# Kernel optimization log

Measured on AMD Instinct MI355X. Metric: run time of the kernel, lower is better.

Reference implementation:

```python
import jax, jax.numpy as jnp
import numpy as np

C_LEN, Q_LEN, D = 8192, 1024, 1024  # D = 2*hidden_size


def setup_inputs() -> dict:
    key = jax.random.key(0)
    ks = jax.random.split(key, 5)
    scale = 1.0 / np.sqrt(D)
    return {
        "H": jax.random.normal(ks[0], (C_LEN, D), dtype=jnp.float32),
        "U": jax.random.normal(ks[1], (Q_LEN, D), dtype=jnp.float32),
        "w_q": jax.random.normal(ks[2], (D,), dtype=jnp.float32) * scale,
        "b_q": jnp.zeros((1,), dtype=jnp.float32),
        "w_c": jax.random.normal(ks[3], (D,), dtype=jnp.float32) * scale,
        "b_c": jnp.zeros((1,), dtype=jnp.float32),
        "w_qc": jax.random.normal(ks[4], (D,), dtype=jnp.float32) * scale,
        "b_qc": jnp.zeros((1,), dtype=jnp.float32),
    }


def reference(H, U, w_q, b_q, w_c, b_c, w_qc, b_qc):
    # Per-token loop qc[:, i] = (H * U[i]) @ w_qc + b_qc collapses to one GEMM:
    # qc[j, i] = sum_k H[j,k] * w_qc[k] * U[i,k] + b_qc
    qc = jnp.einsum("cd,qd->cq", H * w_qc, U) + b_qc          # [c_len, q_len]
    q_term = (U @ w_q + b_q)[None, :]                          # [1, q_len]
    c_term = (H @ w_c + b_c)[:, None]                          # [c_len, 1]
    s = qc + q_term + c_term                                    # [c_len, q_len]
    q2c_atten = jax.nn.softmax(s, axis=0)                       # softmax over context dim (as written)
    U_toggler = q2c_atten @ U                                   # [c_len, D]
    b = jnp.max(H, axis=1)                                      # [c_len]
    c2q_atten = jax.nn.softmax(b)                               # [c_len]
    H_toggler = jnp.broadcast_to((c2q_atten @ H)[None, :], (H.shape[0], H.shape[1]))
    return (U_toggler, H_toggler)
```

## Files before the change

### kernel.cpp

```cpp
#include <hip/hip_runtime.h>

#define C_LEN 8192
#define Q_LEN 1024
#define DDIM  1024

typedef __attribute__((ext_vector_type(8))) short short8;
typedef __attribute__((ext_vector_type(4))) float f32x4;

static __device__ __forceinline__ unsigned short f2bf(float f){
  unsigned u = __float_as_uint(f);
  unsigned rounding = 0x7fffu + ((u >> 16) & 1u);
  return (unsigned short)((u + rounding) >> 16);
}

static __device__ __forceinline__ void async_copy16(const void* g, void* l){
  __builtin_amdgcn_global_load_lds(
      (const __attribute__((address_space(1))) void*)g,
      (__attribute__((address_space(3))) void*)l, 16, 0, 0);
}

static __device__ __forceinline__ float waveRedSum(float v){
  #pragma unroll
  for(int o=32;o;o>>=1) v += __shfl_down(v,o);
  return v;
}
static __device__ __forceinline__ float waveRedMax(float v){
  #pragma unroll
  for(int o=32;o;o>>=1) v = fmaxf(v,__shfl_down(v,o));
  return v;
}

__global__ void prep_H(const float* __restrict__ H, const float* __restrict__ w_qc,
                       const float* __restrict__ w_c, const float* __restrict__ b_c,
                       unsigned short* __restrict__ Abf, float* __restrict__ c_term,
                       float* __restrict__ eb){
  const int c = blockIdx.x, t = threadIdx.x;
  float4 h   = reinterpret_cast<const float4*>(H + (size_t)c*DDIM)[t];
  float4 wqc = reinterpret_cast<const float4*>(w_qc)[t];
  float4 wc  = reinterpret_cast<const float4*>(w_c)[t];
  float dot = h.x*wc.x + h.y*wc.y + h.z*wc.z + h.w*wc.w;
  float mx  = fmaxf(fmaxf(h.x,h.y), fmaxf(h.z,h.w));
  ushort4 o;
  o.x=f2bf(h.x*wqc.x); o.y=f2bf(h.y*wqc.y); o.z=f2bf(h.z*wqc.z); o.w=f2bf(h.w*wqc.w);
  reinterpret_cast<ushort4*>(Abf)[(size_t)c*256 + t] = o;
  __shared__ float sd[4], sm[4];
  int w=t>>6, l=t&63;
  dot = waveRedSum(dot); mx = waveRedMax(mx);
  if(l==0){ sd[w]=dot; sm[w]=mx; }
  __syncthreads();
  if(t==0){
    c_term[c] = sd[0]+sd[1]+sd[2]+sd[3] + b_c[0];
    float m = fmaxf(fmaxf(sm[0],sm[1]), fmaxf(sm[2],sm[3]));
    eb[c] = __expf(m);
  }
}

__global__ void sum_eb(const float* __restrict__ eb, float* __restrict__ btot){
  __shared__ float red[16];
  int t = threadIdx.x, w = t>>6, l = t&63;
  float s = eb[t] + eb[t + 1024] + eb[t + 2048] + eb[t + 3072]
          + eb[t + 4096] + eb[t + 5120] + eb[t + 6144] + eb[t + 7168];
  s = waveRedSum(s);
  if(!l) red[w] = s;
  __syncthreads();
  if(t==0){ float tot=0.f; for(int i=0;i<16;i++) tot+=red[i]; btot[0]=tot; }
}

__global__ void prep_U(const float* __restrict__ U, const float* __restrict__ w_q,
                       const float* __restrict__ b_q, unsigned short* __restrict__ Ubf,
                       float* __restrict__ q_term){
  const int qr = blockIdx.x, t = threadIdx.x;
  float4 u  = reinterpret_cast<const float4*>(U + (size_t)qr*DDIM)[t];
  float4 wq = reinterpret_cast<const float4*>(w_q)[t];
  float dot = u.x*wq.x + u.y*wq.y + u.z*wq.z + u.w*wq.w;
  ushort4 o; o.x=f2bf(u.x); o.y=f2bf(u.y); o.z=f2bf(u.z); o.w=f2bf(u.w);
  reinterpret_cast<ushort4*>(Ubf)[(size_t)qr*256 + t] = o;
  __shared__ float sd[4];
  int w=t>>6, l=t&63;
  dot = waveRedSum(dot);
  if(l==0) sd[w]=dot;
  __syncthreads();
  if(t==0) q_term[qr] = sd[0]+sd[1]+sd[2]+sd[3] + b_q[0];
}

__global__ void transpose_scale_U(const float* __restrict__ U, const float* __restrict__ csum,
                                  unsigned short* __restrict__ Ut){
  __shared__ float tile[64][65];
  const int t = threadIdx.x;
  const int q0 = blockIdx.y*64, d0 = blockIdx.x*64;
  #pragma unroll
  for(int i=0;i<16;i++){
    int idx = i*256 + t, r = idx>>6, col = idx&63;
    tile[r][col] = U[(size_t)(q0+r)*DDIM + d0 + col];
  }
  float inv = 1.f / csum[q0 + (t&63)];
  __syncthreads();
  #pragma unroll
  for(int i=0;i<16;i++){
    int idx = i*256 + t, r = idx>>6, col = idx&63;
    Ut[(size_t)(d0+r)*Q_LEN + q0 + col] = f2bf(tile[col][r] * inv);
  }
}

template<int FUSE_EXP>
__global__ __launch_bounds__(256)
void gemm_bt(const unsigned short* __restrict__ A, const unsigned short* __restrict__ B,
             void* __restrict__ Cout, int M, int N, int K,
             const float* __restrict__ rowAdd, const float* __restrict__ colAdd,
             const float* __restrict__ addC, float* __restrict__ csum){
  __shared__ unsigned short As[2][128][32];
  __shared__ unsigned short Bs[2][128][32];
  const int t = threadIdx.x;
  const int lane = t & 63, wave = t >> 6;
  const int wm = wave & 1, wn = wave >> 1;
  const int lr = lane & 15, quad = lane >> 4;
  const int bm = blockIdx.x * 128, bn = blockIdx.y * 128;
  const int srow = wave*32 + (lane>>2);
  const int skcol = (lane&3)*8;

  f32x4 acc[4][4];
  #pragma unroll
  for(int i=0;i<4;i++)
    #pragma unroll
    for(int j=0;j<4;j++) acc[i][j] = (f32x4){0.f,0.f,0.f,0.f};

  const unsigned short* gA = A + (size_t)(bm + srow)*K + skcol;
  const unsigned short* gB = B + (size_t)(bn + srow)*K + skcol;
  unsigned short* lA[2] = { &As[0][srow][skcol], &As[1][srow][skcol] };
  unsigned short* lB[2] = { &Bs[0][srow][skcol], &Bs[1][srow][skcol] };

  async_copy16(gA,                lA[0]);
  async_copy16(gA + (size_t)16*K, lA[0] + 16*32);
  async_copy16(gB,                lB[0]);
  async_copy16(gB + (size_t)16*K, lB[0] + 16*32);
  gA += 32; gB += 32;

  const int ITERS = K >> 5;
  for(int k=0;k<ITERS;k++){
    const int cur = k & 1, nxt = cur ^ 1;
    __syncthreads();
    if(k+1 < ITERS){
      async_copy16(gA,                lA[nxt]);
      async_copy16(gA + (size_t)16*K, lA[nxt] + 16*32);
      async_copy16(gB,                lB[nxt]);
      async_copy16(gB + (size_t)16*K, lB[nxt] + 16*32);
      gA += 32; gB += 32;
    }
    short8 af[4], bfr[4];
    #pragma unroll
    for(int i=0;i<4;i++){
      af[i]  = *reinterpret_cast<const short8*>(&As[cur][wm*64 + i*16 + lr][quad*8]);
      bfr[i] = *reinterpret_cast<const short8*>(&Bs[cur][wn*64 + i*16 + lr][quad*8]);
    }
    #pragma unroll
    for(int i=0;i<4;i++)
      #pragma unroll
      for(int j=0;j<4;j++)
        acc[i][j] = __builtin_amdgcn_mfma_f32_16x16x32_bf16(af[i], bfr[j], acc[i][j], 0,0,0);
  }

  const int col0 = bn + wn*64;
  if(FUSE_EXP){
    unsigned short* P = (unsigned short*)Cout;
    const float ac = addC[0];
    float cs[4];
    #pragma unroll
    for(int j=0;j<4;j++) cs[j] = 0.f;
    #pragma unroll
    for(int i=0;i<4;i++){
      int row0 = bm + wm*64 + i*16 + quad*4;
      float ra0 = rowAdd[row0], ra1 = rowAdd[row0+1], ra2 = rowAdd[row0+2], ra3 = rowAdd[row0+3];
      #pragma unroll
      for(int j=0;j<4;j++){
        int col = col0 + j*16 + lr;
        float cadd = colAdd[col] + ac;
        float e0 = __expf(acc[i][j][0] + ra0 + cadd);
        float e1 = __expf(acc[i][j][1] + ra1 + cadd);
        float e2 = __expf(acc[i][j][2] + ra2 + cadd);
        float e3 = __expf(acc[i][j][3] + ra3 + cadd);
        P[(size_t)(row0  )*N + col] = f2bf(e0);
        P[(size_t)(row0+1)*N + col] = f2bf(e1);
        P[(size_t)(row0+2)*N + col] = f2bf(e2);
        P[(size_t)(row0+3)*N + col] = f2bf(e3);
        cs[j] += e0+e1+e2+e3;
      }
    }
    #pragma unroll
    for(int j=0;j<4;j++){
      float v = cs[j];
      v += __shfl_xor(v, 16);
      v += __shfl_xor(v, 32);
      if(quad==0) atomicAdd(&csum[col0 + j*16 + lr], v);
    }
  } else {
    float* C = (float*)Cout;
    #pragma unroll
    for(int i=0;i<4;i++){
      int row0 = bm + wm*64 + i*16 + quad*4;
      #pragma unroll
      for(int j=0;j<4;j++){
        int col = col0 + j*16 + lr;
        #pragma unroll
        for(int r=0;r<4;r++)
          C[(size_t)(row0+r)*N + col] = acc[i][j][r];
      }
    }
  }
}

__global__ void h_weighted(const float* __restrict__ H, const float* __restrict__ eb,
                           const float* __restrict__ btot, float* __restrict__ Hrow){
  int d  = blockIdx.x*256 + threadIdx.x;
  int c0 = blockIdx.y*256;
  float acc = 0.f;
  for(int c=c0;c<c0+256;c++)
    acc += eb[c] * H[(size_t)c*DDIM + d];
  atomicAdd(&Hrow[d], acc * (1.f/btot[0]));
}

__global__ void bcast_H(const float* __restrict__ Hrow, float4* __restrict__ out4){
  int gid = blockIdx.x*256 + threadIdx.x;
  int d4 = gid & 255;
  out4[gid] = reinterpret_cast<const float4*>(Hrow)[d4];
}

extern "C" void kernel_launch(void* const* d_in, const int* in_sizes, int n_in,
                              void* d_out, int out_size, void* d_ws, size_t ws_size,
                              hipStream_t stream){
  const float* H    = (const float*)d_in[0];
  const float* U    = (const float*)d_in[1];
  const float* w_q  = (const float*)d_in[2];
  const float* b_q  = (const float*)d_in[3];
  const float* w_c  = (const float*)d_in[4];
  const float* b_c  = (const float*)d_in[5];
  const float* w_qc = (const float*)d_in[6];
  const float* b_qc = (const float*)d_in[7];
  float* out = (float*)d_out;
  char*  ws  = (char*)d_ws;

  unsigned short* P    = (unsigned short*)(ws);
  unsigned short* Abf  = (unsigned short*)(ws + 16777216);
  unsigned short* Ubf  = (unsigned short*)(ws + 33554432);
  unsigned short* Utb  = (unsigned short*)(ws + 35651584);
  char* stats = ws + 37748736;
  float* csum  = (float*)(stats);
  float* Hrow  = (float*)(stats + 4096);
  float* btot  = (float*)(stats + 8192);
  float* cterm = (float*)(stats + 12288);
  float* eb    = (float*)(stats + 45056);
  float* qterm = (float*)(stats + 77824);

  hipMemsetAsync(stats, 0, 8192, stream);

  prep_H<<<C_LEN, 256, 0, stream>>>(H, w_qc, w_c, b_c, Abf, cterm, eb);
  prep_U<<<Q_LEN, 256, 0, stream>>>(U, w_q, b_q, Ubf, qterm);

  gemm_bt<1><<<dim3(64,8), 256, 0, stream>>>(Abf, Ubf, (void*)P, C_LEN, Q_LEN, DDIM,
                                             cterm, qterm, b_qc, csum);

  transpose_scale_U<<<dim3(16,16), 256, 0, stream>>>(U, csum, Utb);

  gemm_bt<0><<<dim3(64,8), 256, 0, stream>>>(P, Utb, (void*)out, C_LEN, DDIM, Q_LEN,
                                             nullptr, nullptr, nullptr, nullptr);

  sum_eb    <<<1, 1024, 0, stream>>>(eb, btot);
  h_weighted<<<dim3(4,32), 256, 0, stream>>>(H, eb, btot, Hrow);
  bcast_H   <<<8192, 256, 0, stream>>>(Hrow, (float4*)(out + (size_t)C_LEN*DDIM));
}
```

Measured before the change: 177.0 us.

## Fuse prep kernels, drop memset and atomics, fold H broadcast into second GEMM

Merges prep_H and prep_U into one launch that also zeroes csum, which removes the memset. It replaces the atomic H-weighted reduction with partial sums plus a combine kernel that also computes the softmax denominator. The broadcast of the H_toggler row now happens in the epilogue of the second GEMM instead of a separate kernel. GEMM tiles are remapped so neighbouring blocks land on the same XCD for L2 reuse. The result is fewer launches and fewer passes over the output, at the cost of a heavier GEMM epilogue.

```diff
diff --git a/kernel.cpp b/kernel.cpp
--- a/kernel.cpp
+++ b/kernel.cpp
@@ -30,57 +30,75 @@
   return v;
 }
 
-__global__ void prep_H(const float* __restrict__ H, const float* __restrict__ w_qc,
-                       const float* __restrict__ w_c, const float* __restrict__ b_c,
-                       unsigned short* __restrict__ Abf, float* __restrict__ c_term,
-                       float* __restrict__ eb){
-  const int c = blockIdx.x, t = threadIdx.x;
-  float4 h   = reinterpret_cast<const float4*>(H + (size_t)c*DDIM)[t];
-  float4 wqc = reinterpret_cast<const float4*>(w_qc)[t];
-  float4 wc  = reinterpret_cast<const float4*>(w_c)[t];
-  float dot = h.x*wc.x + h.y*wc.y + h.z*wc.z + h.w*wc.w;
-  float mx  = fmaxf(fmaxf(h.x,h.y), fmaxf(h.z,h.w));
-  ushort4 o;
-  o.x=f2bf(h.x*wqc.x); o.y=f2bf(h.y*wqc.y); o.z=f2bf(h.z*wqc.z); o.w=f2bf(h.w*wqc.w);
-  reinterpret_cast<ushort4*>(Abf)[(size_t)c*256 + t] = o;
+__global__ void prep_HU(const float* __restrict__ H, const float* __restrict__ U,
+                        const float* __restrict__ w_qc, const float* __restrict__ w_c,
+                        const float* __restrict__ b_c, const float* __restrict__ w_q,
+                        const float* __restrict__ b_q,
+                        unsigned short* __restrict__ Abf, float* __restrict__ cterm,
+                        float* __restrict__ eb, unsigned short* __restrict__ Ubf,
+                        float* __restrict__ qterm, float* __restrict__ csum){
+  const int b = blockIdx.x, t = threadIdx.x;
   __shared__ float sd[4], sm[4];
-  int w=t>>6, l=t&63;
-  dot = waveRedSum(dot); mx = waveRedMax(mx);
-  if(l==0){ sd[w]=dot; sm[w]=mx; }
-  __syncthreads();
-  if(t==0){
-    c_term[c] = sd[0]+sd[1]+sd[2]+sd[3] + b_c[0];
-    float m = fmaxf(fmaxf(sm[0],sm[1]), fmaxf(sm[2],sm[3]));
-    eb[c] = __expf(m);
-  }
-}
-
-__global__ void sum_eb(const float* __restrict__ eb, float* __restrict__ btot){
-  __shared__ float red[16];
+  const int w = t>>6, l = t&63;
+  if(b < C_LEN){
+    float4 h   = reinterpret_cast<const float4*>(H + (size_t)b*DDIM)[t];
+    float4 wqc = reinterpret_cast<const float4*>(w_qc)[t];
+    float4 wc  = reinterpret_cast<const float4*>(w_c)[t];
+    float dot = h.x*wc.x + h.y*wc.y + h.z*wc.z + h.w*wc.w;
+    float mx  = fmaxf(fmaxf(h.x,h.y), fmaxf(h.z,h.w));
+    ushort4 o;
+    o.x=f2bf(h.x*wqc.x); o.y=f2bf(h.y*wqc.y); o.z=f2bf(h.z*wqc.z); o.w=f2bf(h.w*wqc.w);
+    reinterpret_cast<ushort4*>(Abf)[(size_t)b*256 + t] = o;
+    dot = waveRedSum(dot); mx = waveRedMax(mx);
+    if(l==0){ sd[w]=dot; sm[w]=mx; }
+    __syncthreads();
+    if(t==0){
+      cterm[b] = sd[0]+sd[1]+sd[2]+sd[3] + b_c[0];
+      float m = fmaxf(fmaxf(sm[0],sm[1]), fmaxf(sm[2],sm[3]));
+      eb[b] = __expf(m);
+    }
+  } else {
+    const int qr = b - C_LEN;
+    float4 u  = reinterpret_cast<const float4*>(U + (size_t)qr*DDIM)[t];
+    float4 wq = reinterpret_cast<const float4*>(w_q)[t];
+    float dot = u.x*wq.x + u.y*wq.y + u.z*wq.z + u.w*wq.w;
+    ushort4 o; o.x=f2bf(u.x); o.y=f2bf(u.y); o.z=f2bf(u.z); o.w=f2bf(u.w);
+    reinterpret_cast<ushort4*>(Ubf)[(size_t)qr*256 + t] = o;
+    dot = waveRedSum(dot);
+    if(l==0) sd[w]=dot;
+    __syncthreads();
+    if(t==0){
+      qterm[qr] = sd[0]+sd[1]+sd[2]+sd[3] + b_q[0];
+      csum[qr]  = 0.f;
+    }
+  }
+}
+
+__global__ void h_weighted(const float* __restrict__ H, const float* __restrict__ eb,
+                           float* __restrict__ Hpart){
+  int d  = blockIdx.x*256 + threadIdx.x;
+  int cb = blockIdx.y, c0 = cb*256;
+  float acc = 0.f;
+  for(int c=c0;c<c0+256;c++)
+    acc += eb[c] * H[(size_t)c*DDIM + d];
+  Hpart[cb*DDIM + d] = acc;
+}
+
+__global__ void combine_Hrow(const float* __restrict__ Hpart, const float* __restrict__ eb,
+                             float* __restrict__ Hrow){
+  __shared__ float red[4];
   int t = threadIdx.x, w = t>>6, l = t&63;
-  float s = eb[t] + eb[t + 1024] + eb[t + 2048] + eb[t + 3072]
-          + eb[t + 4096] + eb[t + 5120] + eb[t + 6144] + eb[t + 7168];
+  float s = 0.f;
+  for(int i=t;i<C_LEN;i+=256) s += eb[i];
   s = waveRedSum(s);
   if(!l) red[w] = s;
   __syncthreads();
-  if(t==0){ float tot=0.f; for(int i=0;i<16;i++) tot+=red[i]; btot[0]=tot; }
-}
-
-__global__ void prep_U(const float* __restrict__ U, const float* __restrict__ w_q,
-                       const float* __restrict__ b_q, unsigned short* __restrict__ Ubf,
-                       float* __restrict__ q_term){
-  const int qr = blockIdx.x, t = threadIdx.x;
-  float4 u  = reinterpret_cast<const float4*>(U + (size_t)qr*DDIM)[t];
-  float4 wq = reinterpret_cast<const float4*>(w_q)[t];
-  float dot = u.x*wq.x + u.y*wq.y + u.z*wq.z + u.w*wq.w;
-  ushort4 o; o.x=f2bf(u.x); o.y=f2bf(u.y); o.z=f2bf(u.z); o.w=f2bf(u.w);
-  reinterpret_cast<ushort4*>(Ubf)[(size_t)qr*256 + t] = o;
-  __shared__ float sd[4];
-  int w=t>>6, l=t&63;
-  dot = waveRedSum(dot);
-  if(l==0) sd[w]=dot;
-  __syncthreads();
-  if(t==0) q_term[qr] = sd[0]+sd[1]+sd[2]+sd[3] + b_q[0];
+  float btot = red[0]+red[1]+red[2]+red[3];
+  int d = blockIdx.x*256 + t;
+  float acc = 0.f;
+  #pragma unroll
+  for(int p=0;p<32;p++) acc += Hpart[p*DDIM + d];
+  Hrow[d] = acc / btot;
 }
 
 __global__ void transpose_scale_U(const float* __restrict__ U, const float* __restrict__ csum,
@@ -107,14 +125,18 @@
 void gemm_bt(const unsigned short* __restrict__ A, const unsigned short* __restrict__ B,
              void* __restrict__ Cout, int M, int N, int K,
              const float* __restrict__ rowAdd, const float* __restrict__ colAdd,
-             const float* __restrict__ addC, float* __restrict__ csum){
+             const float* __restrict__ addC, float* __restrict__ csum,
+             const float* __restrict__ Hrow, float* __restrict__ outH){
   __shared__ unsigned short As[2][128][32];
   __shared__ unsigned short Bs[2][128][32];
   const int t = threadIdx.x;
   const int lane = t & 63, wave = t >> 6;
   const int wm = wave & 1, wn = wave >> 1;
   const int lr = lane & 15, quad = lane >> 4;
-  const int bm = blockIdx.x * 128, bn = blockIdx.y * 128;
+  const int L = blockIdx.x + (blockIdx.y << 6);
+  const int xcd = L & 7, r = L >> 3;
+  const int by = r & 7, bx = ((r >> 3) << 3) | xcd;
+  const int bm = bx * 128, bn = by * 128;
   const int srow = wave*32 + (lane>>2);
   const int skcol = (lane&3)*8;
 
@@ -205,23 +227,11 @@
           C[(size_t)(row0+r)*N + col] = acc[i][j][r];
       }
     }
-  }
-}
-
-__global__ void h_weighted(const float* __restrict__ H, const float* __restrict__ eb,
-                           const float* __restrict__ btot, float* __restrict__ Hrow){
-  int d  = blockIdx.x*256 + threadIdx.x;
-  int c0 = blockIdx.y*256;
-  float acc = 0.f;
-  for(int c=c0;c<c0+256;c++)
-    acc += eb[c] * H[(size_t)c*DDIM + d];
-  atomicAdd(&Hrow[d], acc * (1.f/btot[0]));
-}
-
-__global__ void bcast_H(const float* __restrict__ Hrow, float4* __restrict__ out4){
-  int gid = blockIdx.x*256 + threadIdx.x;
-  int d4 = gid & 255;
-  out4[gid] = reinterpret_cast<const float4*>(Hrow)[d4];
+    float4 hv = reinterpret_cast<const float4*>(Hrow + bn)[t & 31];
+    #pragma unroll
+    for(int rr = t>>5; rr < 128; rr += 8)
+      reinterpret_cast<float4*>(outH + (size_t)(bm+rr)*DDIM + bn)[t & 31] = hv;
+  }
 }
 
 extern "C" void kernel_launch(void* const* d_in, const int* in_sizes, int n_in,
@@ -245,25 +255,23 @@
   char* stats = ws + 37748736;
   float* csum  = (float*)(stats);
   float* Hrow  = (float*)(stats + 4096);
-  float* btot  = (float*)(stats + 8192);
   float* cterm = (float*)(stats + 12288);
   float* eb    = (float*)(stats + 45056);
   float* qterm = (float*)(stats + 77824);
-
-  hipMemsetAsync(stats, 0, 8192, stream);
-
-  prep_H<<<C_LEN, 256, 0, stream>>>(H, w_qc, w_c, b_c, Abf, cterm, eb);
-  prep_U<<<Q_LEN, 256, 0, stream>>>(U, w_q, b_q, Ubf, qterm);
+  float* Hpart = (float*)(stats + 81920);
+
+  prep_HU<<<C_LEN + Q_LEN, 256, 0, stream>>>(H, U, w_qc, w_c, b_c, w_q, b_q,
+                                             Abf, cterm, eb, Ubf, qterm, csum);
+
+  h_weighted  <<<dim3(4,32), 256, 0, stream>>>(H, eb, Hpart);
+  combine_Hrow<<<4, 256, 0, stream>>>(Hpart, eb, Hrow);
 
   gemm_bt<1><<<dim3(64,8), 256, 0, stream>>>(Abf, Ubf, (void*)P, C_LEN, Q_LEN, DDIM,
-                                             cterm, qterm, b_qc, csum);
+                                             cterm, qterm, b_qc, csum, nullptr, nullptr);
 
   transpose_scale_U<<<dim3(16,16), 256, 0, stream>>>(U, csum, Utb);
 
   gemm_bt<0><<<dim3(64,8), 256, 0, stream>>>(P, Utb, (void*)out, C_LEN, DDIM, Q_LEN,
-                                             nullptr, nullptr, nullptr, nullptr);
-
-  sum_eb    <<<1, 1024, 0, stream>>>(eb, btot);
-  h_weighted<<<dim3(4,32), 256, 0, stream>>>(H, eb, btot, Hrow);
-  bcast_H   <<<8192, 256, 0, stream>>>(Hrow, (float4*)(out + (size_t)C_LEN*DDIM));
-}
+                                             nullptr, nullptr, nullptr, nullptr,
+                                             Hrow, out + (size_t)C_LEN*DDIM);
+}
```

Result: no change. 176.4 us (-0.4%).
